# Kernel tuning notes

Hardware: AMD Instinct MI355X
Metric: run time of the kernel (lower is better)

The kernel has to match this reference:

```python
import jax, jax.numpy as jnp
import numpy as np

V, E, H = 32000, 1024, 1024
T_LEN, B = 70, 64


def _uniform(k, shape, std):
    return jax.random.uniform(k, shape, jnp.float32, -std, std)


def setup_inputs() -> dict:
    key = jax.random.key(0)
    ks = jax.random.split(key, 16)
    x = jax.random.randint(ks[0], (T_LEN, B), 0, V, dtype=jnp.int64)
    h0 = jnp.zeros((3, B, H), jnp.float32)
    c0 = jnp.zeros((3, B, H), jnp.float32)
    emb = jax.random.normal(ks[1], (V, E), jnp.float32)
    s = 1.0 / np.sqrt(H)
    params = {
        'Wi0': _uniform(ks[2], (4 * H, E), s), 'bi0': _uniform(ks[3], (4 * H,), s),
        'Wh0': _uniform(ks[4], (4 * H, H), s), 'bh0': _uniform(ks[5], (4 * H,), s),
        'Wi1': _uniform(ks[6], (4 * H, H), s), 'bi1': _uniform(ks[7], (4 * H,), s),
        'Wh1': _uniform(ks[8], (4 * H, H), s), 'bh1': _uniform(ks[9], (4 * H,), s),
        'Wi2': _uniform(ks[10], (4 * E, H), s), 'bi2': _uniform(ks[11], (4 * E,), s),
        'Wh2': _uniform(ks[12], (4 * E, E), s), 'bh2': _uniform(ks[13], (4 * E,), s),
        'Wd': _uniform(ks[14], (V, E), 0.02), 'bd': jnp.zeros((V,), jnp.float32),
    }
    return {'x': x, 'h0': h0, 'c0': c0, 'emb': emb, **params}


def _cell(px, h, c, Wh, bh, n):
    # px: precomputed input projection [B, 4n]
    p = px + h @ Wh.T + bh
    i = jax.nn.sigmoid(p[:, :n])
    f = jax.nn.sigmoid(p[:, n:2 * n])
    o = jax.nn.sigmoid(p[:, 2 * n:3 * n])   # note: o is 3rd quarter (per source)
    g = jnp.tanh(p[:, 3 * n:])               # g is 4th quarter (per source)
    c2 = f * c + i * g
    h2 = o * jnp.tanh(c2)
    return h2, c2


def reference(x, h0, c0, emb, Wi0, bi0, Wh0, bh0, Wi1, bi1, Wh1, bh1,
              Wi2, bi2, Wh2, bh2, Wd, bd):
    xe = emb[x]                                   # [T, B, E]
    px0 = jnp.einsum('tbe,ge->tbg', xe, Wi0) + bi0  # precompute layer0 input proj

    def step(carry, p0_t):
        (ha, ca, hb, cb, hc, cc) = carry
        ha, ca = _cell(p0_t, ha, ca, Wh0, bh0, H)
        hb, cb = _cell(ha @ Wi1.T + bi1, hb, cb, Wh1, bh1, H)
        hc, cc = _cell(hb @ Wi2.T + bi2, hc, cc, Wh2, bh2, E)
        return (ha, ca, hb, cb, hc, cc), hc

    init = (h0[0], c0[0], h0[1], c0[1], h0[2], c0[2])
    _, out = jax.lax.scan(step, init, px0)        # out: [T, B, E]
    decoded = jnp.einsum('tbe,ve->tbv', out, Wd) + bd  # [T, B, V]
    return decoded
```

## Files before the change

kernel.cpp:

```cpp
#include <hip/hip_runtime.h>

typedef __bf16 bf16;
typedef __bf16 bf16x8 __attribute__((ext_vector_type(8)));
typedef __bf16 bf16x4 __attribute__((ext_vector_type(4)));
typedef float  f32x4  __attribute__((ext_vector_type(4)));
typedef _Float16 f16;
typedef _Float16 f16x8 __attribute__((ext_vector_type(8)));
typedef _Float16 f16x4v __attribute__((ext_vector_type(4)));

#define T_LEN 70
#define BATCH 64
#define HDIM  1024
#define GDIM  4096
#define VOCAB 32000
#define TBROW (T_LEN * BATCH)

#define MFMA16(a, b, c) __builtin_amdgcn_mfma_f32_16x16x32_bf16((a), (b), (c), 0, 0, 0)
#define MFMAH(a, b, c)  __builtin_amdgcn_mfma_f32_16x16x32_f16((a), (b), (c), 0, 0, 0)

typedef const __attribute__((address_space(1))) void gas_void;
typedef __attribute__((address_space(3))) void las_void;

__global__ void split_kernel(const float* __restrict__ w, bf16* __restrict__ hi,
                             bf16* __restrict__ lo, int n4) {
    int stride = gridDim.x * blockDim.x;
    for (int i = blockIdx.x * blockDim.x + threadIdx.x; i < n4; i += stride) {
        float4 v = reinterpret_cast<const float4*>(w)[i];
        bf16 h0 = (bf16)v.x, h1 = (bf16)v.y, h2 = (bf16)v.z, h3 = (bf16)v.w;
        bf16x4 hv = {h0, h1, h2, h3};
        bf16x4 lv = {(bf16)(v.x - (float)h0), (bf16)(v.y - (float)h1),
                     (bf16)(v.z - (float)h2), (bf16)(v.w - (float)h3)};
        reinterpret_cast<bf16x4*>(hi)[i] = hv;
        reinterpret_cast<bf16x4*>(lo)[i] = lv;
    }
}

__global__ void conv_kernel(const float* __restrict__ w, bf16* __restrict__ hi, int n4) {
    int stride = gridDim.x * blockDim.x;
    for (int i = blockIdx.x * blockDim.x + threadIdx.x; i < n4; i += stride) {
        float4 v = reinterpret_cast<const float4*>(w)[i];
        bf16x4 hv = {(bf16)v.x, (bf16)v.y, (bf16)v.z, (bf16)v.w};
        reinterpret_cast<bf16x4*>(hi)[i] = hv;
    }
}

__global__ void conv16_kernel(const float* __restrict__ w, f16* __restrict__ dst, int n4) {
    int stride = gridDim.x * blockDim.x;
    for (int i = blockIdx.x * blockDim.x + threadIdx.x; i < n4; i += stride) {
        float4 v = reinterpret_cast<const float4*>(w)[i];
        f16x4v h = {(f16)v.x, (f16)v.y, (f16)v.z, (f16)v.w};
        reinterpret_cast<f16x4v*>(dst)[i] = h;
    }
}

__global__ void embed_kernel(const int* __restrict__ x, const float* __restrict__ emb,
                             bf16* __restrict__ xh, bf16* __restrict__ xl) {
    int row = blockIdx.x;
    int tok = x[row];
    const float4* src = reinterpret_cast<const float4*>(emb + (size_t)tok * HDIM);
    bf16x4* dh = reinterpret_cast<bf16x4*>(xh + (size_t)row * HDIM);
    bf16x4* dl = reinterpret_cast<bf16x4*>(xl + (size_t)row * HDIM);
    for (int i = threadIdx.x; i < HDIM / 4; i += blockDim.x) {
        float4 v = src[i];
        bf16 h0 = (bf16)v.x, h1 = (bf16)v.y, h2 = (bf16)v.z, h3 = (bf16)v.w;
        dh[i] = (bf16x4){h0, h1, h2, h3};
        dl[i] = (bf16x4){(bf16)(v.x - (float)h0), (bf16)(v.y - (float)h1),
                         (bf16)(v.z - (float)h2), (bf16)(v.w - (float)h3)};
    }
}

__global__ void init16_kernel(const float* __restrict__ h0, f16* __restrict__ hs16) {
    int i = blockIdx.x * blockDim.x + threadIdx.x;
    int l = i >> 16, r = i & 65535;
    hs16[(size_t)(l * 2 + 1) * 65536 + r] = (f16)h0[i];
}

__global__ __launch_bounds__(256) void gemm_bt(
    const bf16* __restrict__ a0, const bf16* __restrict__ a1, const bf16* __restrict__ a2,
    const bf16* __restrict__ b0, const bf16* __restrict__ b1, const bf16* __restrict__ b2,
    int npass, int K, const float* __restrict__ bias, float* __restrict__ C, int ldc) {
    __shared__ __align__(16) char As[128 * 128];
    __shared__ __align__(16) char Bs[128 * 128];
    const int tid = threadIdx.x;
    const int wid = tid >> 6, lane = tid & 63;
    const int l15 = lane & 15, l4 = lane >> 4;

    const int nbx = gridDim.x, mt = gridDim.y, nwg = nbx * mt;
    const int flat = blockIdx.y * nbx + blockIdx.x;
    const int xcd = flat & 7, o8 = flat >> 3;
    const int q8 = nwg >> 3, r8 = nwg & 7;
    const int wg = (xcd < r8 ? xcd * (q8 + 1) : r8 * (q8 + 1) + (xcd - r8) * q8) + o8;
    const int m0 = (wg % mt) * 128, n0 = (wg / mt) * 128;

    const int wr = (wid >> 1) * 64, wc = (wid & 1) * 64;
    const int swz_rd = (l15 & 7) << 4;
    const int rowL = lane >> 3;
    const int colE = (((lane & 7) ^ rowL)) << 3;

    f32x4 acc[4][4];
#pragma unroll
    for (int i = 0; i < 4; ++i)
#pragma unroll
        for (int j = 0; j < 4; ++j) acc[i][j] = (f32x4){0.f, 0.f, 0.f, 0.f};

    for (int p = 0; p < npass; ++p) {
        const bf16* A = (p == 0) ? a0 : ((p == 1) ? a1 : a2);
        const bf16* B = (p == 0) ? b0 : ((p == 1) ? b1 : b2);
        for (int k0 = 0; k0 < K; k0 += 64) {
            __syncthreads();
#pragma unroll
            for (int c2 = 0; c2 < 4; ++c2) {
                const int ch = wid * 4 + c2;
                const int row = ch * 8 + rowL;
                __builtin_amdgcn_global_load_lds(
                    (gas_void*)(A + (size_t)(m0 + row) * K + k0 + colE),
                    (las_void*)(As + ch * 1024), 16, 0, 0);
                __builtin_amdgcn_global_load_lds(
                    (gas_void*)(B + (size_t)(n0 + row) * K + k0 + colE),
                    (las_void*)(Bs + ch * 1024), 16, 0, 0);
            }
            __syncthreads();
#pragma unroll
            for (int ks = 0; ks < 2; ++ks) {
                const int cb = (ks * 64 + l4 * 16) ^ swz_rd;
                bf16x8 af[4], bfr[4];
#pragma unroll
                for (int mi = 0; mi < 4; ++mi)
                    af[mi] = *reinterpret_cast<const bf16x8*>(As + (wr + mi * 16 + l15) * 128 + cb);
#pragma unroll
                for (int ni = 0; ni < 4; ++ni)
                    bfr[ni] = *reinterpret_cast<const bf16x8*>(Bs + (wc + ni * 16 + l15) * 128 + cb);
#pragma unroll
                for (int mi = 0; mi < 4; ++mi)
#pragma unroll
                    for (int ni = 0; ni < 4; ++ni)
                        acc[mi][ni] = MFMA16(af[mi], bfr[ni], acc[mi][ni]);
            }
        }
    }
#pragma unroll
    for (int ni = 0; ni < 4; ++ni) {
        const int col = n0 + wc + ni * 16 + l15;
        const float bv = bias[col];
#pragma unroll
        for (int mi = 0; mi < 4; ++mi) {
            const int row0 = m0 + wr + mi * 16 + l4 * 4;
#pragma unroll
            for (int r = 0; r < 4; ++r)
                C[(size_t)(row0 + r) * ldc + col] = acc[mi][ni][r] + bv;
        }
    }
}

__global__ __launch_bounds__(512, 1) void lstm16(
    const float* __restrict__ cin,
    const f16* __restrict__ W0, const f16* __restrict__ W1, const f16* __restrict__ W2,
    const f16* __restrict__ W3, const f16* __restrict__ W4,
    const float* __restrict__ px0,
    const float* __restrict__ bh0, const float* __restrict__ bi1,
    const float* __restrict__ bh1, const float* __restrict__ bi2,
    const float* __restrict__ bh2,
    f16* __restrict__ hs16, bf16* __restrict__ outh, int* __restrict__ bar,
    f16* __restrict__ dumph, bf16* __restrict__ dumpo) {
    __shared__ __align__(16) char smem[151552];

    const int tid = threadIdx.x;
    const int lane = tid & 63, w = tid >> 6;
    const int l15 = lane & 15, l4 = lane >> 4;
    const int wm = w & 3, wn = w >> 2;
    const int j0 = blockIdx.x * 4;
    const int lq = l15 >> 2;
    const int lcol = lq * 1024 + j0 + (l15 & 3);
    const int lr = lane >> 4;
    const int lp = lane & 15;
    const int ar0 = w * 8 + lr, ar1 = w * 8 + 4 + lr;
    const size_t aoff0 = (size_t)ar0 * HDIM + (size_t)((lp ^ (ar0 & 15)) * 8);
    const size_t aoff1 = (size_t)ar1 * HDIM + (size_t)((lp ^ (ar1 & 15)) * 8);
    const int adst0 = w * 2048, adst1 = w * 2048 + 1024;
    const int crS = (w & 3) * 4 + lr;
    const size_t boffS = (size_t)((crS >> 2) * 1024 + j0 + (crS & 3)) * HDIM +
                         (size_t)((lp ^ crS) * 8);
    const int bdstS = 16384 + ((w & 4) >> 2) * 4096 + (w & 3) * 1024;
    const int a_frow = (wm * 16 + l15) * 256;
    const int b_frow = l15 * 256;
    const int swz_r = l15 << 4;
    const int kbh = wn * 128;
    const int gb = tid >> 2, gj = tid & 3;

    float biasv0 = 0.f, biasv1 = 0.f, biasv2 = 0.f;
    if (wn == 0) {
        biasv0 = bh0[lcol];
        biasv1 = bi1[lcol] + bh1[lcol];
        biasv2 = bi2[lcol] + bh2[lcol];
    }
    float creg0 = 0.f, creg1 = 0.f, creg2 = 0.f;
    if (tid < 256) {
        creg0 = cin[0 * 65536 + gb * 1024 + j0 + gj];
        creg1 = cin[1 * 65536 + gb * 1024 + j0 + gj];
        creg2 = cin[2 * 65536 + gb * 1024 + j0 + gj];
    }

    {
        const f16* wp[3] = {W0, W1, W2};
#pragma unroll
        for (int it = 0; it < 12; ++it) {
            const int u = w * 12 + it;
            const int m = u >> 5, c = (u >> 2) & 7, q = u & 3;
            const int cr = q * 4 + lr;
            const size_t src = (size_t)((cr >> 2) * 1024 + j0 + (cr & 3)) * HDIM +
                               (size_t)(c * 128) + (size_t)((lp ^ cr) * 8);
            __builtin_amdgcn_global_load_lds(
                (gas_void*)(wp[m] + src),
                (las_void*)(smem + m * 32768 + c * 4096 + q * 1024), 16, 0, 0);
        }
    }
    asm volatile("s_waitcnt vmcnt(0) lgkmcnt(0)" ::: "memory");
    __syncthreads();

    auto hsp = [&](int l, int par) { return hs16 + (size_t)(l * 2 + par) * 65536; };

    int barid = 0;

#define WB(N)                                                                    \
    {                                                                            \
        asm volatile("s_waitcnt vmcnt(" #N ")" ::: "memory");                    \
        __builtin_amdgcn_s_barrier();                                            \
        __builtin_amdgcn_sched_barrier(0);                                       \
    }
#define WB2(N0, N1)                                                              \
    {                                                                            \
        if (w < 4) asm volatile("s_waitcnt vmcnt(" #N0 ")" ::: "memory");        \
        else       asm volatile("s_waitcnt vmcnt(" #N1 ")" ::: "memory");        \
        __builtin_amdgcn_s_barrier();                                            \
        __builtin_amdgcn_sched_barrier(0);                                       \
    }
#define CBAR()                                                                   \
    {                                                                            \
        asm volatile("s_waitcnt lgkmcnt(0)" ::: "memory");                       \
        __builtin_amdgcn_s_barrier();                                            \
        __builtin_amdgcn_sched_barrier(0);                                       \
    }

#define ISSUE(c, buf)                                                            \
    {                                                                            \
        const int g_ = ((c) < 8) ? 0 : ((c) < 16) ? 1 : 2;                       \
        const f16* pa_ = (g_ == 0) ? A0 : (g_ == 1) ? A1 : A2;                   \
        const size_t k0_ = (size_t)(((c) & 7) * 128);                            \
        char* base_ = smem + 98304 + (buf) * 24576;                              \
        __builtin_amdgcn_global_load_lds((gas_void*)(pa_ + aoff0 + k0_),         \
                                         (las_void*)(base_ + adst0), 16, 0, 0);  \
        __builtin_amdgcn_global_load_lds((gas_void*)(pa_ + aoff1 + k0_),         \
                                         (las_void*)(base_ + adst1), 16, 0, 0);  \
        if ((c) >= 8) {                                                          \
            const f16* pb_ = ((c) < 16) ? W3 : W4;                               \
            __builtin_amdgcn_global_load_lds((gas_void*)(pb_ + boffS + k0_),     \
                                             (las_void*)(base_ + bdstS), 16, 0, 0); \
        }                                                                        \
    }

#define COMPUTE(buf, cc, G)                                                      \
    {                                                                            \
        const char* base_ = smem + 98304 + (buf) * 24576;                        \
        const char* pin_ = smem + ((G) == 0 ? 0 : 65536) + ((cc) & 7) * 4096;    \
        const char* pin1_ = smem + 32768 + ((cc) & 7) * 4096;                    \
        _Pragma("unroll") for (int ks_ = 0; ks_ < 2; ++ks_) {                    \
            const int kb_ = kbh + ks_ * 64 + l4 * 16;                            \
            const int co_ = kb_ ^ swz_r;                                         \
            f16x8 af_ = *reinterpret_cast<const f16x8*>(base_ + a_frow + co_);   \
            if ((G) == 0) {                                                      \
                f16x8 b0_ = *reinterpret_cast<const f16x8*>(pin_ + b_frow + co_);  \
                f16x8 b1_ = *reinterpret_cast<const f16x8*>(pin1_ + b_frow + co_); \
                if (act0) acc0 = MFMAH(af_, b0_, acc0);                          \
                if (act1) acc1 = MFMAH(af_, b1_, acc1);                          \
            } else if ((G) == 1) {                                               \
                f16x8 b0_ = *reinterpret_cast<const f16x8*>(pin_ + b_frow + co_);  \
                f16x8 b1_ = *reinterpret_cast<const f16x8*>(base_ + 16384 + b_frow + co_); \
                if (act1) acc1 = MFMAH(af_, b0_, acc1);                          \
                if (act2) acc2 = MFMAH(af_, b1_, acc2);                          \
            } else {                                                             \
                f16x8 b0_ = *reinterpret_cast<const f16x8*>(base_ + 16384 + b_frow + co_); \
                if (act2) acc2 = MFMAH(af_, b0_, acc2);                          \
            }                                                                    \
        }                                                                        \
    }

#define EPILOGUE(ACC, BIASV, USEPX, ACT, HD, OH, CREG)                           \
    {                                                                            \
        float* pex = reinterpret_cast<float*>(smem + 147456);                    \
        if (wn == 0) {                                                           \
            _Pragma("unroll") for (int r = 0; r < 4; ++r) {                      \
                const int row = wm * 16 + l4 * 4 + r;                            \
                float v = ACC[r] + (BIASV);                                      \
                if (USEPX) v += pxv[r];                                          \
                pex[row * 16 + l15] = v;                                         \
            }                                                                    \
        }                                                                        \
        CBAR();                                                                  \
        if (wn == 1) {                                                           \
            _Pragma("unroll") for (int r = 0; r < 4; ++r)                        \
                pex[(wm * 16 + l4 * 4 + r) * 16 + l15] += ACC[r];                \
        }                                                                        \
        CBAR();                                                                  \
        if (tid < 256) {                                                         \
            const float pi = pex[gb * 16 + 0 + gj];                              \
            const float pf = pex[gb * 16 + 4 + gj];                              \
            const float po = pex[gb * 16 + 8 + gj];                              \
            const float pg = pex[gb * 16 + 12 + gj];                             \
            const float ig = 1.f / (1.f + expf(-pi));                            \
            const float fg = 1.f / (1.f + expf(-pf));                            \
            const float og = 1.f / (1.f + expf(-po));                            \
            const float gg = tanhf(pg);                                          \
            const float c2v = fg * (CREG) + ig * gg;                             \
            const float h2v = og * tanhf(c2v);                                   \
            if (ACT) (CREG) = c2v;                                               \
            const int idx = gb * 1024 + j0 + gj;                                 \
            (HD)[idx] = (f16)h2v;                                                \
            (OH)[idx] = (bf16)h2v;                                               \
        }                                                                        \
    }

#pragma unroll 1
    for (int s = 0; s < T_LEN + 2; ++s) {
        const int ps = s & 1;
        const bool act0 = (s < T_LEN);
        const bool act1 = (s >= 1) && (s <= T_LEN);
        const bool act2 = (s >= 2);

        const f16* A0 = hsp(0, 1 - ps);
        const f16* A1 = hsp(1, ps);
        const f16* A2 = hsp(2, 1 - ps);
        f16* d0 = act0 ? hsp(0, ps)     : dumph;
        f16* d1 = act1 ? hsp(1, 1 - ps) : dumph;
        f16* d2 = act2 ? hsp(2, ps)     : dumph;
        bf16* ohp = act2 ? (outh + (size_t)(s - 2) * 65536) : dumpo;

        float pxv[4] = {0.f, 0.f, 0.f, 0.f};
        if (wn == 0 && act0) {
            const float* pxr = px0 + (size_t)s * (BATCH * GDIM) +
                               (size_t)(wm * 16 + l4 * 4) * GDIM + lcol;
#pragma unroll
            for (int r = 0; r < 4; ++r) pxv[r] = pxr[(size_t)r * GDIM];
        }

        f32x4 acc0 = (f32x4){0.f, 0.f, 0.f, 0.f};
        f32x4 acc1 = (f32x4){0.f, 0.f, 0.f, 0.f};
        f32x4 acc2 = (f32x4){0.f, 0.f, 0.f, 0.f};

        ISSUE(0, 0) ISSUE(1, 1)

        WB(2) COMPUTE(0, 0, 0) CBAR() ISSUE(2, 0)
        WB(2) COMPUTE(1, 1, 0) CBAR() ISSUE(3, 1)
        WB(2) COMPUTE(0, 2, 0) CBAR() ISSUE(4, 0)
        WB(2) COMPUTE(1, 3, 0) CBAR() ISSUE(5, 1)
        WB(2) COMPUTE(0, 4, 0) CBAR() ISSUE(6, 0)
        WB(2) COMPUTE(1, 5, 0) CBAR() ISSUE(7, 1)
        WB(2) COMPUTE(0, 6, 0) CBAR() ISSUE(8, 0)
        WB(3) COMPUTE(1, 7, 0) CBAR() ISSUE(9, 1)
        EPILOGUE(acc0, biasv0, 1, act0, d0, dumpo, creg0)
        WB2(5, 3) COMPUTE(0, 8, 1)  CBAR() ISSUE(10, 0)
        WB2(5, 3) COMPUTE(1, 9, 1)  CBAR() ISSUE(11, 1)
        WB(3)     COMPUTE(0, 10, 1) CBAR() ISSUE(12, 0)
        WB(3)     COMPUTE(1, 11, 1) CBAR() ISSUE(13, 1)
        WB(3)     COMPUTE(0, 12, 1) CBAR() ISSUE(14, 0)
        WB(3)     COMPUTE(1, 13, 1) CBAR() ISSUE(15, 1)
        WB(3)     COMPUTE(0, 14, 1) CBAR() ISSUE(16, 0)
        WB(3)     COMPUTE(1, 15, 1) CBAR() ISSUE(17, 1)
        EPILOGUE(acc1, biasv1, 0, act1, d1, dumpo, creg1)
        WB2(5, 3) COMPUTE(0, 16, 2) CBAR() ISSUE(18, 0)
        WB2(5, 3) COMPUTE(1, 17, 2) CBAR() ISSUE(19, 1)
        WB(3)     COMPUTE(0, 18, 2) CBAR() ISSUE(20, 0)
        WB(3)     COMPUTE(1, 19, 2) CBAR() ISSUE(21, 1)
        WB(3)     COMPUTE(0, 20, 2) CBAR() ISSUE(22, 0)
        WB(3)     COMPUTE(1, 21, 2) CBAR() ISSUE(23, 1)
        WB(3)     COMPUTE(0, 22, 2) CBAR()
        WB(0)     COMPUTE(1, 23, 2) CBAR()
        EPILOGUE(acc2, biasv2, 0, act2, d2, ohp, creg2)

        if (s < T_LEN + 1) {
            asm volatile("s_waitcnt vmcnt(0) lgkmcnt(0)" ::: "memory");
            __builtin_amdgcn_s_barrier();
            __builtin_amdgcn_sched_barrier(0);
            if (tid == 0) {
                __hip_atomic_fetch_add(&bar[barid], 1, __ATOMIC_RELEASE,
                                       __HIP_MEMORY_SCOPE_AGENT);
                while (__hip_atomic_load(&bar[barid], __ATOMIC_RELAXED,
                                         __HIP_MEMORY_SCOPE_AGENT) < (int)gridDim.x)
                    __builtin_amdgcn_s_sleep(8);
                __builtin_amdgcn_fence(__ATOMIC_ACQUIRE, "agent");
            }
            ++barid;
            __builtin_amdgcn_s_barrier();
            __builtin_amdgcn_sched_barrier(0);
        }
    }
#undef WB
#undef WB2
#undef CBAR
#undef ISSUE
#undef COMPUTE
#undef EPILOGUE
}

extern "C" void kernel_launch(void* const* d_in, const int* in_sizes, int n_in,
                              void* d_out, int out_size, void* d_ws, size_t ws_size,
                              hipStream_t stream) {
    (void)in_sizes; (void)n_in; (void)out_size; (void)ws_size;
    const int*   x   = (const int*)d_in[0];
    const float* h0  = (const float*)d_in[1];
    const float* c0  = (const float*)d_in[2];
    const float* emb = (const float*)d_in[3];
    const float* W[6] = { (const float*)d_in[4],  (const float*)d_in[6],
                          (const float*)d_in[8],  (const float*)d_in[10],
                          (const float*)d_in[12], (const float*)d_in[14] };
    const float* bi0 = (const float*)d_in[5];
    const float* bh0 = (const float*)d_in[7];
    const float* bi1 = (const float*)d_in[9];
    const float* bh1 = (const float*)d_in[11];
    const float* bi2 = (const float*)d_in[13];
    const float* bh2 = (const float*)d_in[15];
    const float* Wd  = (const float*)d_in[16];
    const float* bd  = (const float*)d_in[17];

    char* ws = (char*)d_ws;
    size_t off = 0;
    float* px0 = (float*)(ws + off); off += (size_t)TBROW * GDIM * 4;
    bf16* wsp0 = (bf16*)(ws + off); off += (size_t)GDIM * HDIM * 2;
    bf16* wsp1 = (bf16*)(ws + off); off += (size_t)GDIM * HDIM * 2;
    bf16* wdb  = (bf16*)(ws + off); off += (size_t)VOCAB * HDIM * 2;
    bf16* xeh  = (bf16*)(ws + off); off += (size_t)TBROW * HDIM * 2;
    bf16* xel  = (bf16*)(ws + off); off += (size_t)TBROW * HDIM * 2;
    bf16* outh = (bf16*)(ws + off); off += (size_t)TBROW * HDIM * 2;
    f16* w16[5];
    for (int i = 0; i < 5; ++i) { w16[i] = (f16*)(ws + off); off += (size_t)GDIM * HDIM * 2; }
    f16* hs16  = (f16*)(ws + off); off += (size_t)6 * BATCH * HDIM * 2;
    int* bar   = (int*)(ws + off); off += 1024;
    f16* dumph = (f16*)(ws + off); off += (size_t)BATCH * HDIM * 2;
    bf16* dumpo = (bf16*)(ws + off); off += (size_t)BATCH * HDIM * 2;

    split_kernel<<<1024, 256, 0, stream>>>(W[0], wsp0, wsp1, GDIM * HDIM / 4);
    conv_kernel<<<2048, 256, 0, stream>>>(Wd, wdb, VOCAB * HDIM / 4);
    for (int i = 0; i < 5; ++i)
        conv16_kernel<<<1024, 256, 0, stream>>>(W[i + 1], w16[i], GDIM * HDIM / 4);
    embed_kernel<<<TBROW, 256, 0, stream>>>(x, emb, xeh, xel);
    init16_kernel<<<768, 256, 0, stream>>>(h0, hs16);
    (void)hipMemsetAsync(bar, 0, 1024, stream);

    dim3 gpx(GDIM / 128, TBROW / 128);
    gemm_bt<<<gpx, 256, 0, stream>>>(xeh, xel, xeh, wsp0, wsp0, wsp1,
                                     3, HDIM, bi0, px0, GDIM);

    lstm16<<<256, 512, 0, stream>>>(
        c0, w16[0], w16[1], w16[2], w16[3], w16[4],
        px0, bh0, bi1, bh1, bi2, bh2,
        hs16, outh, bar, dumph, dumpo);

    dim3 gdec(VOCAB / 128, TBROW / 128);
    gemm_bt<<<gdec, 256, 0, stream>>>(outh, nullptr, nullptr, wdb, nullptr, nullptr,
                                      1, HDIM, bd, (float*)d_out, VOCAB);
}
```

Measured before the change: 2.104 ms.

## Triple-buffer LDS staging in LSTM step and drop per-chunk compute barriers

Switches the persistent LSTM kernel's global-to-LDS staging from double to triple buffering (three 20 KB slots instead of two 24 KB slots). This removes the CBAR barrier after each compute chunk, so the next load can be issued into a buffer nobody is reading. The recurrent-weight B tile is now loaded only by waves 0-3 instead of duplicated per wave half, which shrinks each slot. Per-wave vmcnt waits are retuned to match. The risks are higher LDS use (160 KB) and subtle race conditions if the wait counts are off.

Result: no change. 2.065 ms (-1.8%).

```diff
diff --git a/kernel.cpp b/kernel.cpp
--- a/kernel.cpp
+++ b/kernel.cpp
@@ -162,7 +162,7 @@
     const float* __restrict__ bh2,
     f16* __restrict__ hs16, bf16* __restrict__ outh, int* __restrict__ bar,
     f16* __restrict__ dumph, bf16* __restrict__ dumpo) {
-    __shared__ __align__(16) char smem[151552];
+    __shared__ __align__(16) char smem[163840];
 
     const int tid = threadIdx.x;
     const int lane = tid & 63, w = tid >> 6;
@@ -180,7 +180,7 @@
     const int crS = (w & 3) * 4 + lr;
     const size_t boffS = (size_t)((crS >> 2) * 1024 + j0 + (crS & 3)) * HDIM +
                          (size_t)((lp ^ crS) * 8);
-    const int bdstS = 16384 + ((w & 4) >> 2) * 4096 + (w & 3) * 1024;
+    const int bdstS = 16384 + (w & 3) * 1024;
     const int a_frow = (wm * 16 + l15) * 256;
     const int b_frow = l15 * 256;
     const int swz_r = l15 << 4;
@@ -241,17 +241,17 @@
         __builtin_amdgcn_sched_barrier(0);                                       \
     }
 
-#define ISSUE(c, buf)                                                            \
+#define ISSUE(c)                                                                 \
     {                                                                            \
         const int g_ = ((c) < 8) ? 0 : ((c) < 16) ? 1 : 2;                       \
         const f16* pa_ = (g_ == 0) ? A0 : (g_ == 1) ? A1 : A2;                   \
         const size_t k0_ = (size_t)(((c) & 7) * 128);                            \
-        char* base_ = smem + 98304 + (buf) * 24576;                              \
+        char* base_ = smem + 98304 + ((c) % 3) * 20480;                          \
         __builtin_amdgcn_global_load_lds((gas_void*)(pa_ + aoff0 + k0_),         \
                                          (las_void*)(base_ + adst0), 16, 0, 0);  \
         __builtin_amdgcn_global_load_lds((gas_void*)(pa_ + aoff1 + k0_),         \
                                          (las_void*)(base_ + adst1), 16, 0, 0);  \
-        if ((c) >= 8) {                                                          \
+        if ((c) >= 8 && w < 4) {                                                 \
             const f16* pb_ = ((c) < 16) ? W3 : W4;                               \
             __builtin_amdgcn_global_load_lds((gas_void*)(pb_ + boffS + k0_),     \
                                              (las_void*)(base_ + bdstS), 16, 0, 0); \
@@ -260,7 +260,7 @@
 
 #define COMPUTE(buf, cc, G)                                                      \
     {                                                                            \
-        const char* base_ = smem + 98304 + (buf) * 24576;                        \
+        const char* base_ = smem + 98304 + (buf) * 20480;                        \
         const char* pin_ = smem + ((G) == 0 ? 0 : 65536) + ((cc) & 7) * 4096;    \
         const char* pin1_ = smem + 32768 + ((cc) & 7) * 4096;                    \
         _Pragma("unroll") for (int ks_ = 0; ks_ < 2; ++ks_) {                    \
@@ -286,7 +286,7 @@
 
 #define EPILOGUE(ACC, BIASV, USEPX, ACT, HD, OH, CREG)                           \
     {                                                                            \
-        float* pex = reinterpret_cast<float*>(smem + 147456);                    \
+        float* pex = reinterpret_cast<float*>(smem + 159744);                    \
         if (wn == 0) {                                                           \
             _Pragma("unroll") for (int r = 0; r < 4; ++r) {                      \
                 const int row = wm * 16 + l4 * 4 + r;                            \
@@ -346,34 +346,34 @@
         f32x4 acc1 = (f32x4){0.f, 0.f, 0.f, 0.f};
         f32x4 acc2 = (f32x4){0.f, 0.f, 0.f, 0.f};
 
-        ISSUE(0, 0) ISSUE(1, 1)
-
-        WB(2) COMPUTE(0, 0, 0) CBAR() ISSUE(2, 0)
-        WB(2) COMPUTE(1, 1, 0) CBAR() ISSUE(3, 1)
-        WB(2) COMPUTE(0, 2, 0) CBAR() ISSUE(4, 0)
-        WB(2) COMPUTE(1, 3, 0) CBAR() ISSUE(5, 1)
-        WB(2) COMPUTE(0, 4, 0) CBAR() ISSUE(6, 0)
-        WB(2) COMPUTE(1, 5, 0) CBAR() ISSUE(7, 1)
-        WB(2) COMPUTE(0, 6, 0) CBAR() ISSUE(8, 0)
-        WB(3) COMPUTE(1, 7, 0) CBAR() ISSUE(9, 1)
+        ISSUE(0) ISSUE(1) ISSUE(2)
+
+        WB(4)     COMPUTE(0, 0, 0)
+        WB(2)     COMPUTE(1, 1, 0) ISSUE(3)
+        WB(2)     COMPUTE(2, 2, 0) ISSUE(4)
+        WB(2)     COMPUTE(0, 3, 0) ISSUE(5)
+        WB(2)     COMPUTE(1, 4, 0) ISSUE(6)
+        WB(2)     COMPUTE(2, 5, 0) ISSUE(7)
+        WB(2)     COMPUTE(0, 6, 0) ISSUE(8)
+        WB2(3, 2) COMPUTE(1, 7, 0) ISSUE(9)
         EPILOGUE(acc0, biasv0, 1, act0, d0, dumpo, creg0)
-        WB2(5, 3) COMPUTE(0, 8, 1)  CBAR() ISSUE(10, 0)
-        WB2(5, 3) COMPUTE(1, 9, 1)  CBAR() ISSUE(11, 1)
-        WB(3)     COMPUTE(0, 10, 1) CBAR() ISSUE(12, 0)
-        WB(3)     COMPUTE(1, 11, 1) CBAR() ISSUE(13, 1)
-        WB(3)     COMPUTE(0, 12, 1) CBAR() ISSUE(14, 0)
-        WB(3)     COMPUTE(1, 13, 1) CBAR() ISSUE(15, 1)
-        WB(3)     COMPUTE(0, 14, 1) CBAR() ISSUE(16, 0)
-        WB(3)     COMPUTE(1, 15, 1) CBAR() ISSUE(17, 1)
+        WB2(5, 2) COMPUTE(2, 8, 1)  ISSUE(10)
+        WB2(5, 2) COMPUTE(0, 9, 1)  ISSUE(11)
+        WB2(3, 2) COMPUTE(1, 10, 1) ISSUE(12)
+        WB2(3, 2) COMPUTE(2, 11, 1) ISSUE(13)
+        WB2(3, 2) COMPUTE(0, 12, 1) ISSUE(14)
+        WB2(3, 2) COMPUTE(1, 13, 1) ISSUE(15)
+        WB2(3, 2) COMPUTE(2, 14, 1) ISSUE(16)
+        WB2(3, 2) COMPUTE(0, 15, 1) ISSUE(17)
         EPILOGUE(acc1, biasv1, 0, act1, d1, dumpo, creg1)
-        WB2(5, 3) COMPUTE(0, 16, 2) CBAR() ISSUE(18, 0)
-        WB2(5, 3) COMPUTE(1, 17, 2) CBAR() ISSUE(19, 1)
-        WB(3)     COMPUTE(0, 18, 2) CBAR() ISSUE(20, 0)
-        WB(3)     COMPUTE(1, 19, 2) CBAR() ISSUE(21, 1)
-        WB(3)     COMPUTE(0, 20, 2) CBAR() ISSUE(22, 0)
-        WB(3)     COMPUTE(1, 21, 2) CBAR() ISSUE(23, 1)
-        WB(3)     COMPUTE(0, 22, 2) CBAR()
-        WB(0)     COMPUTE(1, 23, 2) CBAR()
+        WB2(5, 2) COMPUTE(1, 16, 2) ISSUE(18)
+        WB2(5, 2) COMPUTE(2, 17, 2) ISSUE(19)
+        WB2(3, 2) COMPUTE(0, 18, 2) ISSUE(20)
+        WB2(3, 2) COMPUTE(1, 19, 2) ISSUE(21)
+        WB2(3, 2) COMPUTE(2, 20, 2) ISSUE(22)
+        WB2(3, 2) COMPUTE(0, 21, 2) ISSUE(23)
+        WB2(3, 2) COMPUTE(1, 22, 2)
+        WB(0)     COMPUTE(2, 23, 2)
         EPILOGUE(acc2, biasv2, 0, act2, d2, ohp, creg2)
 
         if (s < T_LEN + 1) {
```
